# Kernel optimization log

Hardware: AMD Instinct MI355X
Metric: run time of the kernel (lower is better)

Reference implementation:

```python
import jax, jax.numpy as jnp
import numpy as np
from jax import lax

T, IMG, C_IN = 2048, 84, 4
HID = 256
NUM_OUT = 18
FEAT = 6 * 6 * 32  # 84 -> 42 -> 21 -> 11 -> 6 with stride-2 SAME convs


def setup_inputs() -> dict:
    key = jax.random.key(0)
    ks = jax.random.split(key, 8)
    d = {}
    d["x"] = jax.random.normal(ks[0], (T, IMG, IMG, C_IN), jnp.float32)
    cin = C_IN
    for i in range(4):
        d[f"conv_w{i}"] = jax.random.normal(ks[1 + i], (3, 3, cin, 32), jnp.float32) * (1.0 / np.sqrt(9 * cin))
        d[f"conv_b{i}"] = jnp.zeros((32,), jnp.float32)
        cin = 32
    d["lstm_w"] = jax.random.normal(ks[5], (FEAT + HID, 4 * HID), jnp.float32) * (1.0 / np.sqrt(FEAT + HID))
    d["lstm_b"] = jnp.zeros((4 * HID,), jnp.float32)
    d["fc_w"] = jax.random.normal(ks[6], (HID, NUM_OUT), jnp.float32) * 0.01
    d["fc_b"] = jnp.zeros((NUM_OUT,), jnp.float32)
    d["c_in"] = jnp.zeros((1, HID), jnp.float32)
    d["h_in"] = jnp.zeros((1, HID), jnp.float32)
    return d


def _conv_stack(x, ws, bs):
    dn = ("NHWC", "HWIO", "NHWC")
    for w, b in zip(ws, bs):
        x = jax.nn.elu(lax.conv_general_dilated(x, w, (2, 2), "SAME", dimension_numbers=dn) + b)
    return x.reshape(x.shape[0], -1)  # [T, FEAT]


def _lstm(feats, c0, h0, lstm_w, lstm_b):
    # BasicLSTMCell: gates [i, j, f, o], forget_bias = 1.0
    def step(carry, xt):
        c, h = carry  # [1, HID] each
        z = jnp.concatenate([xt[None, :], h], axis=1) @ lstm_w + lstm_b
        i, j, f, o = jnp.split(z, 4, axis=1)
        c = c * jax.nn.sigmoid(f + 1.0) + jax.nn.sigmoid(i) * jnp.tanh(j)
        h = jnp.tanh(c) * jax.nn.sigmoid(o)
        return (c, h), h[0]

    (_, _), hs = lax.scan(step, (c0, h0), feats)
    return hs  # [T, HID]


def reference(x, c_in, h_in,
              conv_w0, conv_b0, conv_w1, conv_b1,
              conv_w2, conv_b2, conv_w3, conv_b3,
              lstm_w, lstm_b, fc_w, fc_b):
    feats = _conv_stack(x, [conv_w0, conv_w1, conv_w2, conv_w3],
                        [conv_b0, conv_b1, conv_b2, conv_b3])
    hs = _lstm(feats, c_in, h_in, lstm_w, lstm_b)
    logits = hs @ fc_w + fc_b  # [T, NUM_OUT]
    return logits, hs
```

## Files before the change

kernel.cpp:

```cpp
#include <hip/hip_runtime.h>
#include <hip/hip_bf16.h>

__device__ inline float fsig(float x) { return 1.0f / (1.0f + __expf(-x)); }
__device__ inline float ftanh(float x) {
    float ax = fabsf(x);
    float e = __expf(-2.0f * ax);
    float r = (1.0f - e) / (1.0f + e);
    return x >= 0.0f ? r : -r;
}
__device__ inline float felu(float x) { return x > 0.0f ? x : expm1f(x); }

typedef _Float16 h2_t __attribute__((ext_vector_type(2)));

__device__ inline unsigned int packh2(float a, float b) {
    unsigned short ua = __builtin_bit_cast(unsigned short, (_Float16)a);
    unsigned short ub = __builtin_bit_cast(unsigned short, (_Float16)b);
    return (unsigned int)ua | ((unsigned int)ub << 16);
}
__device__ inline unsigned short f16bits(float a) {
    return __builtin_bit_cast(unsigned short, (_Float16)a);
}

__device__ inline float dot2acc(unsigned int w, unsigned int h, float acc) {
#if __has_builtin(__builtin_amdgcn_fdot2)
    return __builtin_amdgcn_fdot2(__builtin_bit_cast(h2_t, w), __builtin_bit_cast(h2_t, h), acc, false);
#else
    _Float16 wlo = __builtin_bit_cast(_Float16, (unsigned short)(w & 0xffff));
    _Float16 whi = __builtin_bit_cast(_Float16, (unsigned short)(w >> 16));
    _Float16 hlo = __builtin_bit_cast(_Float16, (unsigned short)(h & 0xffff));
    _Float16 hhi = __builtin_bit_cast(_Float16, (unsigned short)(h >> 16));
    return acc + (float)wlo * (float)hlo + (float)whi * (float)hhi;
#endif
}

__global__ __launch_bounds__(256) void conv0_kernel(const float* __restrict__ in,
                                                    const float* __restrict__ wg,
                                                    const float* __restrict__ bias,
                                                    unsigned short* __restrict__ out) {
    constexpr int W = 84, OW = 42, PAD = 0, WP = W + 2;
    __shared__ float in_s[3 * WP * 4];
    constexpr int NQ = 3 * WP;
    const int tid = threadIdx.x;
    const int oy = blockIdx.x;
    const int t = blockIdx.y;
    const int co = tid & 31;

    for (int q = tid; q < NQ; q += 256) {
        int ky = q / WP;
        int col = q - ky * WP;
        int iy = 2 * oy - PAD + ky;
        int ix = col - 1;
        float4 v = make_float4(0.f, 0.f, 0.f, 0.f);
        if (iy >= 0 && iy < W && ix >= 0 && ix < W)
            v = *(const float4*)&in[(((size_t)t * W + iy) * W + ix) * 4];
        *(float4*)&in_s[q * 4] = v;
    }

    float wr[9][4];
#pragma unroll
    for (int tap = 0; tap < 9; ++tap)
#pragma unroll
        for (int j = 0; j < 4; ++j) wr[tap][j] = wg[(tap * 4 + j) * 32 + co];
    __syncthreads();

    const int g = tid >> 5;
    constexpr int NOX = (OW + 7) / 8;
    float acc[NOX];
#pragma unroll
    for (int m = 0; m < NOX; ++m) acc[m] = 0.f;
#pragma unroll
    for (int ky = 0; ky < 3; ++ky)
#pragma unroll
        for (int kx = 0; kx < 3; ++kx) {
            float w0 = wr[ky * 3 + kx][0], w1 = wr[ky * 3 + kx][1];
            float w2 = wr[ky * 3 + kx][2], w3 = wr[ky * 3 + kx][3];
#pragma unroll
            for (int m = 0; m < NOX; ++m) {
                int ox = g + 8 * m;
                if (ox < OW) {
                    int cs = 2 * ox + kx - PAD + 1;
                    float4 xi = *(const float4*)&in_s[(ky * WP + cs) * 4];
                    acc[m] += xi.x * w0 + xi.y * w1 + xi.z * w2 + xi.w * w3;
                }
            }
        }
    float b = bias[co];
#pragma unroll
    for (int m = 0; m < NOX; ++m) {
        int ox = g + 8 * m;
        if (ox < OW)
            out[(((size_t)t * OW + oy) * OW + ox) * 32 + co] = f16bits(felu(acc[m] + b));
    }
}

template <int W, int OW, int PAD, bool F32OUT>
__global__ __launch_bounds__(256) void convh_kernel(const unsigned short* __restrict__ in,
                                                    const float* __restrict__ wg,
                                                    const float* __restrict__ bias,
                                                    void* __restrict__ outv) {
    constexpr int WP = W + 2;
    constexpr int OWH = (OW + 1) / 2;
    __shared__ __align__(16) unsigned short in_s[3][WP][32];
    __shared__ float zs[4][OW * 32];

    const int tid = threadIdx.x;
    const int oy = blockIdx.x;
    const int t = blockIdx.y;
    const int co = tid & 31;
    const int cig = (tid >> 5) & 3;
    const int oxh = tid >> 7;

    constexpr int NQ4 = 3 * WP * 4;
    uint4* in_s4 = reinterpret_cast<uint4*>(&in_s[0][0][0]);
    for (int q = tid; q < NQ4; q += 256) {
        int ky = q / (WP * 4);
        int rem = q - ky * (WP * 4);
        int col = rem >> 2, c4 = rem & 3;
        int iy = 2 * oy - PAD + ky;
        int ix = col - 1;
        uint4 v = make_uint4(0u, 0u, 0u, 0u);
        if (iy >= 0 && iy < W && ix >= 0 && ix < W)
            v = *(const uint4*)&in[(((size_t)t * W + iy) * W + ix) * 32 + c4 * 8];
        in_s4[q] = v;
    }

    unsigned int wr[9][4];
#pragma unroll
    for (int tap = 0; tap < 9; ++tap)
#pragma unroll
        for (int p = 0; p < 4; ++p)
            wr[tap][p] = packh2(wg[(tap * 32 + cig * 8 + 2 * p) * 32 + co],
                                wg[(tap * 32 + cig * 8 + 2 * p + 1) * 32 + co]);
    __syncthreads();

    float acc[OWH];
#pragma unroll
    for (int m = 0; m < OWH; ++m) acc[m] = 0.f;
#pragma unroll
    for (int ky = 0; ky < 3; ++ky)
#pragma unroll
        for (int kx = 0; kx < 3; ++kx) {
            unsigned int w0 = wr[ky * 3 + kx][0], w1 = wr[ky * 3 + kx][1];
            unsigned int w2 = wr[ky * 3 + kx][2], w3 = wr[ky * 3 + kx][3];
#pragma unroll
            for (int m = 0; m < OWH; ++m) {
                int ox = oxh * OWH + m;
                if (ox < OW) {
                    int cs = 2 * ox + kx - PAD + 1;
                    uint4 h8 = *(const uint4*)&in_s[ky][cs][cig * 8];
                    acc[m] = dot2acc(w0, h8.x, acc[m]);
                    acc[m] = dot2acc(w1, h8.y, acc[m]);
                    acc[m] = dot2acc(w2, h8.z, acc[m]);
                    acc[m] = dot2acc(w3, h8.w, acc[m]);
                }
            }
        }
#pragma unroll
    for (int m = 0; m < OWH; ++m) {
        int ox = oxh * OWH + m;
        if (ox < OW) zs[cig][ox * 32 + co] = acc[m];
    }
    __syncthreads();

    for (int idx = tid; idx < OW * 32; idx += 256) {
        float s = zs[0][idx] + zs[1][idx] + zs[2][idx] + zs[3][idx] + bias[idx & 31];
        s = felu(s);
        if constexpr (F32OUT)
            ((float*)outv)[(((size_t)t * OW + oy) * OW) * 32 + idx] = s;
        else
            ((unsigned short*)outv)[(((size_t)t * OW + oy) * OW) * 32 + idx] = f16bits(s);
    }
}

__global__ void gemm_kernel(const float* __restrict__ A, const float* __restrict__ Wx,
                            const float* __restrict__ bias, float* __restrict__ C) {
    __shared__ float As[32][64];
    __shared__ float Bs[32][64];
    const int bn = blockIdx.x, bm = blockIdx.y;
    const int tx = threadIdx.x, ty = threadIdx.y;
    const int tid = ty * 16 + tx;
    float acc[4][4] = {};
    for (int k0 = 0; k0 < 1152; k0 += 32) {
        {
            int r = tid >> 3;
            int c = (tid & 7) * 4;
            float4 a0 = *(const float4*)&A[(size_t)(bm * 64 + r) * 1152 + k0 + c];
            float4 a1 = *(const float4*)&A[(size_t)(bm * 64 + r + 32) * 1152 + k0 + c];
            As[c + 0][r] = a0.x; As[c + 1][r] = a0.y; As[c + 2][r] = a0.z; As[c + 3][r] = a0.w;
            As[c + 0][r + 32] = a1.x; As[c + 1][r + 32] = a1.y; As[c + 2][r + 32] = a1.z; As[c + 3][r + 32] = a1.w;
            int rb = tid >> 4;
            int cb = (tid & 15) * 4;
            *(float4*)&Bs[rb][cb] = *(const float4*)&Wx[(size_t)(k0 + rb) * 1024 + bn * 64 + cb];
            *(float4*)&Bs[rb + 16][cb] = *(const float4*)&Wx[(size_t)(k0 + rb + 16) * 1024 + bn * 64 + cb];
        }
        __syncthreads();
#pragma unroll
        for (int kk = 0; kk < 32; ++kk) {
            float4 a = *(float4*)&As[kk][ty * 4];
            float4 b = *(float4*)&Bs[kk][tx * 4];
            acc[0][0] += a.x * b.x; acc[0][1] += a.x * b.y; acc[0][2] += a.x * b.z; acc[0][3] += a.x * b.w;
            acc[1][0] += a.y * b.x; acc[1][1] += a.y * b.y; acc[1][2] += a.y * b.z; acc[1][3] += a.y * b.w;
            acc[2][0] += a.z * b.x; acc[2][1] += a.z * b.y; acc[2][2] += a.z * b.z; acc[2][3] += a.z * b.w;
            acc[3][0] += a.w * b.x; acc[3][1] += a.w * b.y; acc[3][2] += a.w * b.z; acc[3][3] += a.w * b.w;
        }
        __syncthreads();
    }
#pragma unroll
    for (int i = 0; i < 4; ++i) {
        int row = bm * 64 + ty * 4 + i;
#pragma unroll
        for (int j = 0; j < 4; ++j) {
            int col = bn * 64 + tx * 4 + j;
            C[(size_t)row * 1024 + col] = acc[i][j] + bias[col];
        }
    }
}

__global__ __launch_bounds__(512, 2) void lstm4_kernel(const float* __restrict__ lstm_w,
                                                       const float* __restrict__ xpart,
                                                       const float* __restrict__ c_in,
                                                       const float* __restrict__ h_in,
                                                       float* __restrict__ hs_out) {
    __shared__ __align__(16) unsigned int wlds[1024][36];
    __shared__ float zsm[1024];
    __shared__ __align__(16) unsigned short hbuf[2][256];

    const int tid = threadIdx.x;
    const int c0 = tid;
    const int c1 = tid + 512;

    for (int p = 0; p < 32; ++p) {
        wlds[c0][p] = packh2(lstm_w[(size_t)(1152 + 2 * p) * 1024 + c0],
                             lstm_w[(size_t)(1152 + 2 * p + 1) * 1024 + c0]);
        wlds[c1][p] = packh2(lstm_w[(size_t)(1152 + 2 * p) * 1024 + c1],
                             lstm_w[(size_t)(1152 + 2 * p + 1) * 1024 + c1]);
    }
    unsigned int wrA[96], wrB[96];
#pragma unroll
    for (int r = 0; r < 96; ++r) {
        int p = 32 + r;
        wrA[r] = packh2(lstm_w[(size_t)(1152 + 2 * p) * 1024 + c0],
                        lstm_w[(size_t)(1152 + 2 * p + 1) * 1024 + c0]);
        wrB[r] = packh2(lstm_w[(size_t)(1152 + 2 * p) * 1024 + c1],
                        lstm_w[(size_t)(1152 + 2 * p + 1) * 1024 + c1]);
    }

    float c_state = 0.0f;
    if (tid < 256) {
        c_state = c_in[tid];
        hbuf[0][tid] = f16bits(h_in[tid]);
    }
    __syncthreads();

    float xpA = xpart[c0];
    float xpB = xpart[c1];
    for (int t = 0; t < 2048; ++t) {
        const int cur = t & 1;
        const uint4* hq = reinterpret_cast<const uint4*>(&hbuf[cur][0]);

        float a0 = 0.f, a1 = 0.f, a2 = 0.f, a3 = 0.f;
        float b0 = 0.f, b1 = 0.f, b2 = 0.f, b3 = 0.f;
#pragma unroll
        for (int c = 0; c < 8; ++c) {
            uint4 h4 = hq[c];
            uint4 wa = *reinterpret_cast<const uint4*>(&wlds[c0][4 * c]);
            uint4 wb = *reinterpret_cast<const uint4*>(&wlds[c1][4 * c]);
            a0 = dot2acc(wa.x, h4.x, a0); a1 = dot2acc(wa.y, h4.y, a1);
            a2 = dot2acc(wa.z, h4.z, a2); a3 = dot2acc(wa.w, h4.w, a3);
            b0 = dot2acc(wb.x, h4.x, b0); b1 = dot2acc(wb.y, h4.y, b1);
            b2 = dot2acc(wb.z, h4.z, b2); b3 = dot2acc(wb.w, h4.w, b3);
        }
#pragma unroll
        for (int c = 8; c < 32; ++c) {
            uint4 h4 = hq[c];
            const int r = 4 * c - 32;
            a0 = dot2acc(wrA[r + 0], h4.x, a0); a1 = dot2acc(wrA[r + 1], h4.y, a1);
            a2 = dot2acc(wrA[r + 2], h4.z, a2); a3 = dot2acc(wrA[r + 3], h4.w, a3);
            b0 = dot2acc(wrB[r + 0], h4.x, b0); b1 = dot2acc(wrB[r + 1], h4.y, b1);
            b2 = dot2acc(wrB[r + 2], h4.z, b2); b3 = dot2acc(wrB[r + 3], h4.w, b3);
        }
        zsm[c0] = (a0 + a1) + (a2 + a3) + xpA;
        zsm[c1] = (b0 + b1) + (b2 + b3) + xpB;

        float xpAn = 0.f, xpBn = 0.f;
        if (t + 1 < 2048) {
            xpAn = xpart[(size_t)(t + 1) * 1024 + c0];
            xpBn = xpart[(size_t)(t + 1) * 1024 + c1];
        }

        asm volatile("s_waitcnt lgkmcnt(0)\n\ts_barrier" ::: "memory");

        if (tid < 256) {
            float zi = zsm[tid];
            float zg = zsm[256 + tid];
            float zf = zsm[512 + tid];
            float zo = zsm[768 + tid];
            c_state = c_state * fsig(zf + 1.0f) + fsig(zi) * ftanh(zg);
            float h = ftanh(c_state) * fsig(zo);
            hs_out[(size_t)t * 256 + tid] = h;
            hbuf[cur ^ 1][tid] = f16bits(h);
        }

        asm volatile("s_waitcnt lgkmcnt(0)\n\ts_barrier" ::: "memory");
        xpA = xpAn;
        xpB = xpBn;
    }
}

__global__ void logits_kernel(const float* __restrict__ hs, const float* __restrict__ fc_w,
                              const float* __restrict__ fc_b, float* __restrict__ out) {
    int idx = blockIdx.x * 256 + threadIdx.x;
    if (idx >= 2048 * 18) return;
    int t = idx / 18, n = idx % 18;
    float acc = fc_b[n];
    const float* hrow = hs + (size_t)t * 256;
#pragma unroll 4
    for (int k = 0; k < 256; ++k) acc += hrow[k] * fc_w[k * 18 + n];
    out[idx] = acc;
}

extern "C" void kernel_launch(void* const* d_in, const int* in_sizes, int n_in,
                              void* d_out, int out_size, void* d_ws, size_t ws_size,
                              hipStream_t stream) {
    const float* x   = (const float*)d_in[0];
    const float* w0  = (const float*)d_in[1];
    const float* b0  = (const float*)d_in[2];
    const float* w1  = (const float*)d_in[3];
    const float* b1  = (const float*)d_in[4];
    const float* w2  = (const float*)d_in[5];
    const float* b2  = (const float*)d_in[6];
    const float* w3  = (const float*)d_in[7];
    const float* b3  = (const float*)d_in[8];
    const float* lw  = (const float*)d_in[9];
    const float* lb  = (const float*)d_in[10];
    const float* fcw = (const float*)d_in[11];
    const float* fcb = (const float*)d_in[12];
    const float* cin = (const float*)d_in[13];
    const float* hin = (const float*)d_in[14];

    float* outp = (float*)d_out;
    float* hs_out = outp + 2048 * 18;

    const size_t FIXED_B = ((size_t)2048 * 1152 + (size_t)2048 * 1024) * 4;
    const size_t PERT_B = ((size_t)56448 + 14112 + 3872) * 2;

    int C = 128;
    const int cands[5] = {2048, 1024, 512, 256, 128};
    for (int i = 0; i < 5; ++i) {
        if (FIXED_B + (size_t)cands[i] * PERT_B <= ws_size) { C = cands[i]; break; }
    }

    float* feats = (float*)d_ws;
    float* xpart = feats + (size_t)2048 * 1152;
    unsigned short* c0buf = (unsigned short*)(xpart + (size_t)2048 * 1024);
    unsigned short* c1buf = c0buf + (size_t)C * 56448;
    unsigned short* c2buf = c1buf + (size_t)C * 14112;

    for (int t0 = 0; t0 < 2048; t0 += C) {
        const float* xin = x + (size_t)t0 * 84 * 84 * 4;
        conv0_kernel<<<dim3(42, C), 256, 0, stream>>>(xin, w0, b0, c0buf);
        convh_kernel<42, 21, 0, false><<<dim3(21, C), 256, 0, stream>>>(c0buf, w1, b1, c1buf);
        convh_kernel<21, 11, 1, false><<<dim3(11, C), 256, 0, stream>>>(c1buf, w2, b2, c2buf);
        convh_kernel<11, 6, 1, true><<<dim3(6, C), 256, 0, stream>>>(c2buf, w3, b3,
                                                                     feats + (size_t)t0 * 1152);
    }

    gemm_kernel<<<dim3(16, 32), dim3(16, 16), 0, stream>>>(feats, lw, lb, xpart);
    lstm4_kernel<<<1, 512, 0, stream>>>(lw, xpart, cin, hin, hs_out);
    logits_kernel<<<144, 256, 0, stream>>>(hs_out, fcw, fcb, outp);
}
```

Before: 4.561 ms.

## Split LSTM recurrent dot products along K across thread halves

Reworks the single-block LSTM recurrence. Each thread now owns one hidden unit's four gates over half of the 256-long hidden vector, rather than two full gate columns. The two partial sums are reduced through shared memory, and every thread computes the cell update redundantly so the post-barrier gate reads need no extra gathering. The register-resident weight slice grows and VGPR use is pinned to 256, which trades occupancy and spill risk for a shorter per-step serial dependency chain.

```diff
diff --git a/kernel.cpp b/kernel.cpp
--- a/kernel.cpp
+++ b/kernel.cpp
@@ -216,94 +216,103 @@
     }
 }
 
-__global__ __launch_bounds__(512, 2) void lstm4_kernel(const float* __restrict__ lstm_w,
-                                                       const float* __restrict__ xpart,
-                                                       const float* __restrict__ c_in,
-                                                       const float* __restrict__ h_in,
-                                                       float* __restrict__ hs_out) {
-    __shared__ __align__(16) unsigned int wlds[1024][36];
-    __shared__ float zsm[1024];
-    __shared__ __align__(16) unsigned short hbuf[2][256];
+__global__ __attribute__((amdgpu_flat_work_group_size(512, 512), amdgpu_num_vgpr(256)))
+void lstm7_kernel(const float* __restrict__ lstm_w,
+                  const float* __restrict__ xpart,
+                  const float* __restrict__ c_in,
+                  const float* __restrict__ h_in,
+                  float* __restrict__ hs_out) {
+    __shared__ __align__(16) unsigned int wl[512][52];
+    __shared__ float zsm[2][4][256];
+    __shared__ __align__(16) unsigned int hpk[2][2][68];
 
     const int tid = threadIdx.x;
-    const int c0 = tid;
-    const int c1 = tid + 512;
-
-    for (int p = 0; p < 32; ++p) {
-        wlds[c0][p] = packh2(lstm_w[(size_t)(1152 + 2 * p) * 1024 + c0],
-                             lstm_w[(size_t)(1152 + 2 * p + 1) * 1024 + c0]);
-        wlds[c1][p] = packh2(lstm_w[(size_t)(1152 + 2 * p) * 1024 + c1],
-                             lstm_w[(size_t)(1152 + 2 * p + 1) * 1024 + c1]);
-    }
-    unsigned int wrA[96], wrB[96];
-#pragma unroll
-    for (int r = 0; r < 96; ++r) {
-        int p = 32 + r;
-        wrA[r] = packh2(lstm_w[(size_t)(1152 + 2 * p) * 1024 + c0],
-                        lstm_w[(size_t)(1152 + 2 * p + 1) * 1024 + c0]);
-        wrB[r] = packh2(lstm_w[(size_t)(1152 + 2 * p) * 1024 + c1],
-                        lstm_w[(size_t)(1152 + 2 * p + 1) * 1024 + c1]);
-    }
-
-    float c_state = 0.0f;
+    const int s = tid >> 8;
+    const int u = tid & 255;
+
+    for (int q = 0; q < 4; ++q)
+        for (int p = 0; p < 12; ++p) {
+            int gp = 64 * s + p;
+            wl[tid][q * 12 + p] = packh2(lstm_w[(size_t)(1152 + 2 * gp) * 1024 + 256 * q + u],
+                                         lstm_w[(size_t)(1152 + 2 * gp + 1) * 1024 + 256 * q + u]);
+        }
+    unsigned int wreg[4][52];
+#pragma unroll
+    for (int q = 0; q < 4; ++q)
+        for (int p = 12; p < 64; ++p) {
+            int gp = 64 * s + p;
+            wreg[q][p - 12] = packh2(lstm_w[(size_t)(1152 + 2 * gp) * 1024 + 256 * q + u],
+                                     lstm_w[(size_t)(1152 + 2 * gp + 1) * 1024 + 256 * q + u]);
+        }
+
+    float c_state = c_in[u];
     if (tid < 256) {
-        c_state = c_in[tid];
-        hbuf[0][tid] = f16bits(h_in[tid]);
+        unsigned short* hrow = (unsigned short*)&hpk[0][u >> 7][0];
+        hrow[u & 127] = f16bits(h_in[u]);
     }
     __syncthreads();
 
-    float xpA = xpart[c0];
-    float xpB = xpart[c1];
+    float xp0 = xpart[u], xp1 = xpart[256 + u], xp2 = xpart[512 + u], xp3 = xpart[768 + u];
+
     for (int t = 0; t < 2048; ++t) {
         const int cur = t & 1;
-        const uint4* hq = reinterpret_cast<const uint4*>(&hbuf[cur][0]);
-
-        float a0 = 0.f, a1 = 0.f, a2 = 0.f, a3 = 0.f;
-        float b0 = 0.f, b1 = 0.f, b2 = 0.f, b3 = 0.f;
-#pragma unroll
-        for (int c = 0; c < 8; ++c) {
+        const uint4* hq = reinterpret_cast<const uint4*>(&hpk[cur][s][0]);
+
+        float acc[4] = {0.f, 0.f, 0.f, 0.f};
+        {
+            uint4 hA = hq[0], hB = hq[1], hC = hq[2];
+#pragma unroll
+            for (int q = 0; q < 4; ++q) {
+                uint4 wa = *(const uint4*)&wl[tid][q * 12];
+                uint4 wb = *(const uint4*)&wl[tid][q * 12 + 4];
+                uint4 wc = *(const uint4*)&wl[tid][q * 12 + 8];
+                acc[q] = dot2acc(wa.x, hA.x, acc[q]); acc[q] = dot2acc(wa.y, hA.y, acc[q]);
+                acc[q] = dot2acc(wa.z, hA.z, acc[q]); acc[q] = dot2acc(wa.w, hA.w, acc[q]);
+                acc[q] = dot2acc(wb.x, hB.x, acc[q]); acc[q] = dot2acc(wb.y, hB.y, acc[q]);
+                acc[q] = dot2acc(wb.z, hB.z, acc[q]); acc[q] = dot2acc(wb.w, hB.w, acc[q]);
+                acc[q] = dot2acc(wc.x, hC.x, acc[q]); acc[q] = dot2acc(wc.y, hC.y, acc[q]);
+                acc[q] = dot2acc(wc.z, hC.z, acc[q]); acc[q] = dot2acc(wc.w, hC.w, acc[q]);
+            }
+        }
+#pragma unroll
+        for (int c = 3; c < 16; ++c) {
             uint4 h4 = hq[c];
-            uint4 wa = *reinterpret_cast<const uint4*>(&wlds[c0][4 * c]);
-            uint4 wb = *reinterpret_cast<const uint4*>(&wlds[c1][4 * c]);
-            a0 = dot2acc(wa.x, h4.x, a0); a1 = dot2acc(wa.y, h4.y, a1);
-            a2 = dot2acc(wa.z, h4.z, a2); a3 = dot2acc(wa.w, h4.w, a3);
-            b0 = dot2acc(wb.x, h4.x, b0); b1 = dot2acc(wb.y, h4.y, b1);
-            b2 = dot2acc(wb.z, h4.z, b2); b3 = dot2acc(wb.w, h4.w, b3);
-        }
-#pragma unroll
-        for (int c = 8; c < 32; ++c) {
-            uint4 h4 = hq[c];
-            const int r = 4 * c - 32;
-            a0 = dot2acc(wrA[r + 0], h4.x, a0); a1 = dot2acc(wrA[r + 1], h4.y, a1);
-            a2 = dot2acc(wrA[r + 2], h4.z, a2); a3 = dot2acc(wrA[r + 3], h4.w, a3);
-            b0 = dot2acc(wrB[r + 0], h4.x, b0); b1 = dot2acc(wrB[r + 1], h4.y, b1);
-            b2 = dot2acc(wrB[r + 2], h4.z, b2); b3 = dot2acc(wrB[r + 3], h4.w, b3);
-        }
-        zsm[c0] = (a0 + a1) + (a2 + a3) + xpA;
-        zsm[c1] = (b0 + b1) + (b2 + b3) + xpB;
-
-        float xpAn = 0.f, xpBn = 0.f;
+            const int r = 4 * (c - 3);
+#pragma unroll
+            for (int q = 0; q < 4; ++q) {
+                acc[q] = dot2acc(wreg[q][r + 0], h4.x, acc[q]);
+                acc[q] = dot2acc(wreg[q][r + 1], h4.y, acc[q]);
+                acc[q] = dot2acc(wreg[q][r + 2], h4.z, acc[q]);
+                acc[q] = dot2acc(wreg[q][r + 3], h4.w, acc[q]);
+            }
+        }
+        zsm[s][0][u] = acc[0];
+        zsm[s][1][u] = acc[1];
+        zsm[s][2][u] = acc[2];
+        zsm[s][3][u] = acc[3];
+
+        float xn0 = 0.f, xn1 = 0.f, xn2 = 0.f, xn3 = 0.f;
         if (t + 1 < 2048) {
-            xpAn = xpart[(size_t)(t + 1) * 1024 + c0];
-            xpBn = xpart[(size_t)(t + 1) * 1024 + c1];
+            const float* xr = &xpart[(size_t)(t + 1) * 1024];
+            xn0 = xr[u]; xn1 = xr[256 + u]; xn2 = xr[512 + u]; xn3 = xr[768 + u];
         }
 
         asm volatile("s_waitcnt lgkmcnt(0)\n\ts_barrier" ::: "memory");
 
+        float zi = zsm[0][0][u] + zsm[1][0][u] + xp0;
+        float zj = zsm[0][1][u] + zsm[1][1][u] + xp1;
+        float zf = zsm[0][2][u] + zsm[1][2][u] + xp2;
+        float zo = zsm[0][3][u] + zsm[1][3][u] + xp3;
+        c_state = c_state * fsig(zf + 1.0f) + fsig(zi) * ftanh(zj);
+        float h = ftanh(c_state) * fsig(zo);
         if (tid < 256) {
-            float zi = zsm[tid];
-            float zg = zsm[256 + tid];
-            float zf = zsm[512 + tid];
-            float zo = zsm[768 + tid];
-            c_state = c_state * fsig(zf + 1.0f) + fsig(zi) * ftanh(zg);
-            float h = ftanh(c_state) * fsig(zo);
-            hs_out[(size_t)t * 256 + tid] = h;
-            hbuf[cur ^ 1][tid] = f16bits(h);
+            hs_out[(size_t)t * 256 + u] = h;
+            unsigned short* hrow = (unsigned short*)&hpk[cur ^ 1][u >> 7][0];
+            hrow[u & 127] = f16bits(h);
         }
 
         asm volatile("s_waitcnt lgkmcnt(0)\n\ts_barrier" ::: "memory");
-        xpA = xpAn;
-        xpB = xpBn;
+        xp0 = xn0; xp1 = xn1; xp2 = xn2; xp3 = xn3;
     }
 }
 
@@ -366,6 +375,6 @@
     }
 
     gemm_kernel<<<dim3(16, 32), dim3(16, 16), 0, stream>>>(feats, lw, lb, xpart);
-    lstm4_kernel<<<1, 512, 0, stream>>>(lw, xpart, cin, hin, hs_out);
+    lstm7_kernel<<<1, 512, 0, stream>>>(lw, xpart, cin, hin, hs_out);
     logits_kernel<<<144, 256, 0, stream>>>(hs_out, fcw, fcb, outp);
 }
```

Measured after the change: 4.262 ms (median of 2 runs). 6.6% less time.
